# Performance work log

Hardware: AMD Instinct MI355X
Metric: run time of the kernel (lower is better)

## Reference

```python
import jax, jax.numpy as jnp
import numpy as np
import math

IN_DIMS, OUT_DIMS, N = 128, 32, 2048
B, O = 64, 8
LN_EPS = 1e-5


def setup_inputs() -> dict:
    key = jax.random.key(0)
    k_x, k_w = jax.random.split(key)
    x = jax.random.normal(k_x, (B, O, N, IN_DIMS), dtype=jnp.float32)
    bound = 1.0 / math.sqrt(IN_DIMS + OUT_DIMS)
    w1 = jax.random.uniform(k_w, (IN_DIMS, OUT_DIMS, N), dtype=jnp.float32,
                            minval=-bound, maxval=bound)
    b1 = jnp.zeros((1, N, OUT_DIMS), dtype=jnp.float32)
    T = jnp.array([1.0], dtype=jnp.float32)
    gamma = jnp.ones((IN_DIMS,), dtype=jnp.float32)
    beta = jnp.zeros((IN_DIMS,), dtype=jnp.float32)
    return {"x": x, "w1": w1, "b1": b1, "T": T, "gamma": gamma, "beta": beta}


def reference(x, w1, b1, T, gamma, beta):
    # dropout=0 -> identity. LayerNorm over last (in_dims) axis, affine.
    mu = jnp.mean(x, axis=-1, keepdims=True)
    var = jnp.mean(jnp.square(x - mu), axis=-1, keepdims=True)
    h = (x - mu) * jax.lax.rsqrt(var + LN_EPS) * gamma + beta
    # per-position (N) grouped linear: x[b,o,d,m] @ w1[m,h,d] -> [b,o,d,h]
    out = jnp.einsum('BODM,MHD->BODH', h, w1) + b1  # b1 (1,N,H) broadcasts over B,O
    # torch squeeze(-1) is a no-op since out_dims > 1
    return out / T
```

## Files before the change

### kernel.cpp

```cpp
#include <hip/hip_runtime.h>
#include <stdint.h>

#define NPOS 2048
#define LN_EPS 1e-5f

typedef short short8 __attribute__((ext_vector_type(8)));
typedef float floatx4 __attribute__((ext_vector_type(4)));

__device__ __forceinline__ uint32_t bf16_rne(float f) {
  uint32_t u = __float_as_uint(f);
  return (u + 0x7fffu + ((u >> 16) & 1u)) >> 16;
}
__device__ __forceinline__ uint32_t pack2(float lo, float hi) {
  return bf16_rne(lo) | (bf16_rne(hi) << 16);
}

__global__ __launch_bounds__(256) void superlinear_kernel(
    const float* __restrict__ x,
    const float* __restrict__ w1,
    const float* __restrict__ b1,
    const float* __restrict__ T,
    const float* __restrict__ gamma,
    const float* __restrict__ beta,
    float* __restrict__ out)
{
  __shared__ uint4 Xs[32 * 64];
  __shared__ uint4 Gs[8 * 64];
  __shared__ float2 stats[128];
  __shared__ __align__(16) float gam[128];
  __shared__ __align__(16) float bet[128];
  __shared__ float c1s[32], es[32];

  const int d = blockIdx.x;
  const int t = threadIdx.x;
  const float invT = 1.0f / T[0];

  if (t < 32)      ((float4*)gam)[t]      = ((const float4*)gamma)[t];
  else if (t < 64) ((float4*)bet)[t - 32] = ((const float4*)beta)[t - 32];

  {
    const int region = t >> 5;
    const int ktile = region >> 1, ht = region & 1;
#pragma unroll
    for (int cc = 0; cc < 2; ++cc) {
      const int cw = ((t & 31) << 1) | cc;
      const int kq = cw >> 4, n = cw & 15;
      const int h = ht * 16 + n;
      const int mb = ktile * 32 + kq * 8;
      const float* wp = w1 + (size_t)mb * (32 * NPOS) + (size_t)h * NPOS + d;
      uint4 v;
      v.x = pack2(wp[0 * 65536], wp[1 * 65536]);
      v.y = pack2(wp[2 * 65536], wp[3 * 65536]);
      v.z = pack2(wp[4 * 65536], wp[5 * 65536]);
      v.w = pack2(wp[6 * 65536], wp[7 * 65536]);
      Gs[region * 64 + cw] = v;
    }
  }
  __syncthreads();

  if (t < 32) {
    const int ht = t >> 4, n = t & 15;
    const unsigned short* Gu = (const unsigned short*)Gs;
    float c1 = 0.f, c2 = 0.f;
#pragma unroll 8
    for (int m = 0; m < 128; ++m) {
      const int ktile = m >> 5, kq = (m >> 3) & 3, j = m & 7;
      const float w = __uint_as_float((uint32_t)Gu[(ktile * 2 + ht) * 512 + (kq * 16 + n) * 8 + j] << 16);
      c1 = fmaf(gam[m], w, c1);
      c2 = fmaf(bet[m], w, c2);
    }
    c1s[t] = c1;
    es[t] = (c2 + b1[d * 32 + t]) * invT;
  }

  const int c0 = (t & 15) * 8;
  const float4 ga = ((const float4*)(gam + c0))[0];
  const float4 gb = ((const float4*)(gam + c0))[1];

  const int wv = t >> 6, L = t & 63, quad = L >> 4;
  const short8* Gs8 = (const short8*)Gs;
  const short8* Xs8 = (const short8*)Xs;

  for (int ti = 0; ti < 4; ++ti) {
    const int r16 = t >> 4;
#pragma unroll
    for (int it = 0; it < 8; ++it) {
      const int lrow = it * 16 + r16;
      const float* xp = x + (size_t)(ti * 128 + lrow) * (NPOS * 128) + (size_t)d * 128 + c0;
      const float4 xa = ((const float4*)xp)[0];
      const float4 xb = ((const float4*)xp)[1];
      float s1 = xa.x + xa.y + xa.z + xa.w + xb.x + xb.y + xb.z + xb.w;
      float s2 = xa.x * xa.x + xa.y * xa.y + xa.z * xa.z + xa.w * xa.w
               + xb.x * xb.x + xb.y * xb.y + xb.z * xb.z + xb.w * xb.w;
#pragma unroll
      for (int msk = 1; msk < 16; msk <<= 1) {
        s1 += __shfl_xor(s1, msk, 64);
        s2 += __shfl_xor(s2, msk, 64);
      }
      if ((t & 15) == 0) {
        const float mu = s1 * (1.0f / 128.f);
        const float var = fmaf(-mu, mu, s2 * (1.0f / 128.f));
        const float rs = rsqrtf(var + LN_EPS);
        stats[lrow] = make_float2(rs * invT, mu * rs * invT);
      }
      uint4 v;
      v.x = pack2(xa.x * ga.x, xa.y * ga.y);
      v.y = pack2(xa.z * ga.z, xa.w * ga.w);
      v.z = pack2(xb.x * gb.x, xb.y * gb.y);
      v.w = pack2(xb.z * gb.z, xb.w * gb.w);
      const int ktile = (t & 15) >> 2, k8 = t & 3;
      const int c = k8 * 16 + r16;
      const int p = c ^ (k8 << 1) ^ ((ktile & 1) << 2) ^ (ktile >> 1);
      Xs[(it * 4 + ktile) * 64 + p] = v;
    }
    __syncthreads();

#pragma unroll
    for (int ht = 0; ht < 2; ++ht) {
      short8 bfr[4];
#pragma unroll
      for (int kt = 0; kt < 4; ++kt) bfr[kt] = Gs8[(kt * 2 + ht) * 64 + L];
      const int h = ht * 16 + (L & 15);
      const float c1v = c1s[h], ev = es[h];
#pragma unroll
      for (int rt = 0; rt < 2; ++rt) {
        const int rtile = wv * 2 + rt;
        floatx4 acc = {0.f, 0.f, 0.f, 0.f};
#pragma unroll
        for (int kt = 0; kt < 4; ++kt) {
          const int p = L ^ ((L >> 4) << 1) ^ ((kt & 1) << 2) ^ (kt >> 1);
          const short8 afr = Xs8[(rtile * 4 + kt) * 64 + p];
          acc = __builtin_amdgcn_mfma_f32_16x16x32_bf16(afr, bfr[kt], acc, 0, 0, 0);
        }
        const int lr0 = rtile * 16 + quad * 4;
#pragma unroll
        for (int r = 0; r < 4; ++r) {
          const float2 st = stats[lr0 + r];
          const float val = fmaf(st.x, acc[r], fmaf(-st.y, c1v, ev));
          out[(size_t)(ti * 128 + lr0 + r) * (NPOS * 32) + (size_t)d * 32 + h] = val;
        }
      }
    }
    __syncthreads();
  }
}

extern "C" void kernel_launch(void* const* d_in, const int* in_sizes, int n_in,
                              void* d_out, int out_size, void* d_ws, size_t ws_size,
                              hipStream_t stream) {
  const float* x     = (const float*)d_in[0];
  const float* w1    = (const float*)d_in[1];
  const float* b1    = (const float*)d_in[2];
  const float* T     = (const float*)d_in[3];
  const float* gamma = (const float*)d_in[4];
  const float* beta  = (const float*)d_in[5];
  float* out = (float*)d_out;
  hipLaunchKernelGGL(superlinear_kernel, dim3(NPOS), dim3(256), 0, stream,
                     x, w1, b1, T, gamma, beta, out);
}
```

Baseline: 787.6 us.

## Pre-pack weights and LN correction terms in separate kernels before main fused kernel

Splits the per-position weight work out of the main kernel. One pre-pass repacks w1 into bf16 MFMA-fragment order in workspace with coalesced reads along d, and another computes the gamma/beta-weighted column sums and the bias term. The main kernel then does a contiguous 8KB load of the packed weights and reads the precomputed c1/e values straight from global memory. It drops the strided weight gather, the serial 32-thread reduction, and some shared memory, and adds an occupancy hint of 3 blocks. The cost is two extra launches and extra workspace traffic, and c1 is now computed from fp32 weights rather than bf16-rounded ones.

```diff
diff --git a/kernel.cpp b/kernel.cpp
--- a/kernel.cpp
+++ b/kernel.cpp
@@ -1,4 +1,5 @@
 #include <hip/hip_runtime.h>
+#include <hip/hip_bf16.h>
 #include <stdint.h>
 
 #define NPOS 2048
@@ -7,77 +8,93 @@
 typedef short short8 __attribute__((ext_vector_type(8)));
 typedef float floatx4 __attribute__((ext_vector_type(4)));
 
-__device__ __forceinline__ uint32_t bf16_rne(float f) {
-  uint32_t u = __float_as_uint(f);
-  return (u + 0x7fffu + ((u >> 16) & 1u)) >> 16;
-}
-__device__ __forceinline__ uint32_t pack2(float lo, float hi) {
-  return bf16_rne(lo) | (bf16_rne(hi) << 16);
+__device__ __forceinline__ uint32_t packbf2(float lo, float hi) {
+  __hip_bfloat162 h = __float22bfloat162_rn(make_float2(lo, hi));
+  uint32_t u;
+  __builtin_memcpy(&u, &h, 4);
+  return u;
 }
 
-__global__ __launch_bounds__(256) void superlinear_kernel(
+__global__ __launch_bounds__(256) void wpack_kernel(
+    const float* __restrict__ w1, uint4* __restrict__ wp)
+{
+  const int dlane = threadIdx.x & 63;
+  const int sub   = threadIdx.x >> 6;
+  const int dg    = blockIdx.x >> 4;
+  const int cg    = blockIdx.x & 15;
+  const int d     = dg * 64 + dlane;
+#pragma unroll
+  for (int i = 0; i < 8; ++i) {
+    const int chunkid = (cg * 4 + sub) * 8 + i;
+    const int region = chunkid >> 6, chunk = chunkid & 63;
+    const int ktile = region >> 1, ht = region & 1;
+    const int kq = chunk >> 4, n = chunk & 15;
+    const int h  = ht * 16 + n;
+    const int mb = ktile * 32 + kq * 8;
+    const float* src = w1 + (size_t)mb * (32 * NPOS) + (size_t)h * NPOS + d;
+    uint4 v;
+    v.x = packbf2(src[0 * 65536], src[1 * 65536]);
+    v.y = packbf2(src[2 * 65536], src[3 * 65536]);
+    v.z = packbf2(src[4 * 65536], src[5 * 65536]);
+    v.w = packbf2(src[6 * 65536], src[7 * 65536]);
+    wp[(size_t)d * 512 + chunkid] = v;
+  }
+}
+
+__global__ __launch_bounds__(256) void c12_kernel(
+    const float* __restrict__ w1, const float* __restrict__ b1,
+    const float* __restrict__ T, const float* __restrict__ gamma,
+    const float* __restrict__ beta,
+    float* __restrict__ c1g, float* __restrict__ eg)
+{
+  const int tid = blockIdx.x * 256 + threadIdx.x;
+  const int d = tid & (NPOS - 1);
+  const int h = tid >> 11;
+  float c1 = 0.f, c2 = 0.f;
+#pragma unroll 8
+  for (int m = 0; m < 128; ++m) {
+    const float w = w1[(size_t)(m * 32 + h) * NPOS + d];
+    c1 = fmaf(gamma[m], w, c1);
+    c2 = fmaf(beta[m], w, c2);
+  }
+  c1g[tid] = c1;
+  eg[tid] = (c2 + b1[d * 32 + h]) / T[0];
+}
+
+__global__ __launch_bounds__(256, 3) void superlinear_kernel(
     const float* __restrict__ x,
-    const float* __restrict__ w1,
-    const float* __restrict__ b1,
+    const uint4* __restrict__ wp,
+    const float* __restrict__ c1g,
+    const float* __restrict__ eg,
     const float* __restrict__ T,
     const float* __restrict__ gamma,
-    const float* __restrict__ beta,
     float* __restrict__ out)
 {
   __shared__ uint4 Xs[32 * 64];
   __shared__ uint4 Gs[8 * 64];
   __shared__ float2 stats[128];
-  __shared__ __align__(16) float gam[128];
-  __shared__ __align__(16) float bet[128];
-  __shared__ float c1s[32], es[32];
 
   const int d = blockIdx.x;
   const int t = threadIdx.x;
   const float invT = 1.0f / T[0];
 
-  if (t < 32)      ((float4*)gam)[t]      = ((const float4*)gamma)[t];
-  else if (t < 64) ((float4*)bet)[t - 32] = ((const float4*)beta)[t - 32];
-
   {
-    const int region = t >> 5;
-    const int ktile = region >> 1, ht = region & 1;
-#pragma unroll
-    for (int cc = 0; cc < 2; ++cc) {
-      const int cw = ((t & 31) << 1) | cc;
-      const int kq = cw >> 4, n = cw & 15;
-      const int h = ht * 16 + n;
-      const int mb = ktile * 32 + kq * 8;
-      const float* wp = w1 + (size_t)mb * (32 * NPOS) + (size_t)h * NPOS + d;
-      uint4 v;
-      v.x = pack2(wp[0 * 65536], wp[1 * 65536]);
-      v.y = pack2(wp[2 * 65536], wp[3 * 65536]);
-      v.z = pack2(wp[4 * 65536], wp[5 * 65536]);
-      v.w = pack2(wp[6 * 65536], wp[7 * 65536]);
-      Gs[region * 64 + cw] = v;
-    }
-  }
-  __syncthreads();
-
-  if (t < 32) {
-    const int ht = t >> 4, n = t & 15;
-    const unsigned short* Gu = (const unsigned short*)Gs;
-    float c1 = 0.f, c2 = 0.f;
-#pragma unroll 8
-    for (int m = 0; m < 128; ++m) {
-      const int ktile = m >> 5, kq = (m >> 3) & 3, j = m & 7;
-      const float w = __uint_as_float((uint32_t)Gu[(ktile * 2 + ht) * 512 + (kq * 16 + n) * 8 + j] << 16);
-      c1 = fmaf(gam[m], w, c1);
-      c2 = fmaf(bet[m], w, c2);
-    }
-    c1s[t] = c1;
-    es[t] = (c2 + b1[d * 32 + t]) * invT;
+    const uint4* src = wp + (size_t)d * 512;
+    Gs[t]       = src[t];
+    Gs[t + 256] = src[t + 256];
   }
 
   const int c0 = (t & 15) * 8;
-  const float4 ga = ((const float4*)(gam + c0))[0];
-  const float4 gb = ((const float4*)(gam + c0))[1];
+  const float4 ga = ((const float4*)(gamma + c0))[0];
+  const float4 gb = ((const float4*)(gamma + c0))[1];
 
   const int wv = t >> 6, L = t & 63, quad = L >> 4;
+  const int hA = L & 15;
+  const float c1r0 = c1g[hA * NPOS + d];
+  const float c1r1 = c1g[(hA + 16) * NPOS + d];
+  const float er0  = eg[hA * NPOS + d];
+  const float er1  = eg[(hA + 16) * NPOS + d];
+
   const short8* Gs8 = (const short8*)Gs;
   const short8* Xs8 = (const short8*)Xs;
 
@@ -104,10 +121,10 @@
         stats[lrow] = make_float2(rs * invT, mu * rs * invT);
       }
       uint4 v;
-      v.x = pack2(xa.x * ga.x, xa.y * ga.y);
-      v.y = pack2(xa.z * ga.z, xa.w * ga.w);
-      v.z = pack2(xb.x * gb.x, xb.y * gb.y);
-      v.w = pack2(xb.z * gb.z, xb.w * gb.w);
+      v.x = packbf2(xa.x * ga.x, xa.y * ga.y);
+      v.y = packbf2(xa.z * ga.z, xa.w * ga.w);
+      v.z = packbf2(xb.x * gb.x, xb.y * gb.y);
+      v.w = packbf2(xb.z * gb.z, xb.w * gb.w);
       const int ktile = (t & 15) >> 2, k8 = t & 3;
       const int c = k8 * 16 + r16;
       const int p = c ^ (k8 << 1) ^ ((ktile & 1) << 2) ^ (ktile >> 1);
@@ -120,8 +137,9 @@
       short8 bfr[4];
 #pragma unroll
       for (int kt = 0; kt < 4; ++kt) bfr[kt] = Gs8[(kt * 2 + ht) * 64 + L];
-      const int h = ht * 16 + (L & 15);
-      const float c1v = c1s[h], ev = es[h];
+      const int h = ht * 16 + hA;
+      const float c1v = ht ? c1r1 : c1r0;
+      const float ev  = ht ? er1 : er0;
 #pragma unroll
       for (int rt = 0; rt < 2; ++rt) {
         const int rtile = wv * 2 + rt;
@@ -155,6 +173,14 @@
   const float* gamma = (const float*)d_in[4];
   const float* beta  = (const float*)d_in[5];
   float* out = (float*)d_out;
+
+  uint4* wp  = (uint4*)d_ws;
+  float* c1g = (float*)((char*)d_ws + (size_t)16 * 1024 * 1024);
+  float* eg  = (float*)((char*)d_ws + (size_t)16 * 1024 * 1024 + 256 * 1024);
+
+  hipLaunchKernelGGL(wpack_kernel, dim3(512), dim3(256), 0, stream, w1, wp);
+  hipLaunchKernelGGL(c12_kernel, dim3(256), dim3(256), 0, stream,
+                     w1, b1, T, gamma, beta, c1g, eg);
   hipLaunchKernelGGL(superlinear_kernel, dim3(NPOS), dim3(256), 0, stream,
-                     x, w1, b1, T, gamma, beta, out);
+                     x, wp, c1g, eg, T, gamma, out);
 }
```

New measurement: 778.2 us. Within noise of the previous version (-1.2%).
